# Performance work log

Hardware: AMD Instinct MI355X
Metric: run time of the kernel (lower is better)

The kernel has to match this reference:

```python
import jax, jax.numpy as jnp
import numpy as np

B, N, D, F, L, R = 16, 1024, 256, 128, 2, 2


def setup_inputs() -> dict:
    key = jax.random.key(0)
    ks = jax.random.split(key, 12)
    s = 0.05
    return {
        "node_embed": jax.random.normal(ks[0], (B, N, D), jnp.float32),
        "input_x": jax.random.normal(ks[1], (B, F), jnp.float32),
        "adj": jax.random.randint(ks[2], (R, B, N, N), 0, 2, jnp.int32),
        "WQi_w": jax.random.normal(ks[3], (L, F, F), jnp.float32) * s,
        "WQi_b": jnp.zeros((L, F), jnp.float32),
        "WQ_w": jax.random.normal(ks[4], (L, D + F, D), jnp.float32) * s,
        "WQ_b": jnp.zeros((L, D), jnp.float32),
        "WK_w": jax.random.normal(ks[5], (L, R, D + F, D), jnp.float32) * s,
        "WK_b": jnp.zeros((L, R, D), jnp.float32),
        "WV_w": jax.random.normal(ks[6], (L, R, D + F, D), jnp.float32) * s,
        "WV_b": jnp.zeros((L, R, D), jnp.float32),
        "WF_w": jax.random.normal(ks[7], (L, R * D, D), jnp.float32) * s,
        "WF_b": jnp.zeros((L, D), jnp.float32),
        "ln_g": jnp.ones((L, D), jnp.float32),
        "ln_b": jnp.zeros((L, D), jnp.float32),
    }


def _layer_norm(x, g, b, eps=1e-5):
    mu = jnp.mean(x, axis=-1, keepdims=True)
    var = jnp.var(x, axis=-1, keepdims=True)
    return (x - mu) * jax.lax.rsqrt(var + eps) * g + b


def reference(node_embed, input_x, adj, WQi_w, WQi_b, WQ_w, WQ_b,
              WK_w, WK_b, WV_w, WV_b, WF_w, WF_b, ln_g, ln_b):
    scale = 1.0 / (D ** 0.5)
    h = node_embed
    for l in range(L):
        # input feature projection, broadcast over nodes
        x1 = input_x @ WQi_w[l] + WQi_b[l]              # (B, F)
        x1 = jnp.broadcast_to(x1[:, None, :], (h.shape[0], h.shape[1], F))
        qc = jnp.concatenate([h, x1], axis=-1)          # (B, N, D+F)
        q = qc @ WQ_w[l] + WQ_b[l]                      # (B, N, D)
        outs = []
        for r in range(R):
            k = qc @ WK_w[l, r] + WK_b[l, r]            # (B, N, D)
            v = qc @ WV_w[l, r] + WV_b[l, r]            # (B, N, D)
            scores = jnp.einsum('bnd,bmd->bnm', q, k) * scale
            scores = jnp.where(adj[r] == 0, -1e9, scores)
            alpha = jax.nn.softmax(scores, axis=-1)
            outs.append(jnp.einsum('bnm,bmd->bnd', alpha, v))
        h_concat = jnp.concatenate(outs, axis=-1)       # (B, N, R*D)
        h_fused = jax.nn.relu(h_concat @ WF_w[l] + WF_b[l])
        h = _layer_norm(h + h_fused, ln_g[l], ln_b[l])
    return h
```

## Files before the change

kernel.cpp:

```cpp
#include <hip/hip_runtime.h>
#include <hip/hip_bf16.h>

#define BB 16
#define NN 1024
#define DD 256
#define FF_ 128
#define LL 2
#define RR 2
#define DF 384
#define MM (BB*NN)
#define NPROJ 1280
#define PK 768

typedef __attribute__((ext_vector_type(8))) short s16x8;
typedef __attribute__((ext_vector_type(4))) float f32x4;
typedef __attribute__((ext_vector_type(4))) unsigned short us16x4;

__device__ __forceinline__ unsigned short f2bf(float f){
  unsigned u = __builtin_bit_cast(unsigned, f);
  u += 0x7fff + ((u >> 16) & 1);
  return (unsigned short)(u >> 16);
}

__device__ __forceinline__ void gload16(const void* g, void* l){
  __builtin_amdgcn_global_load_lds(
      (const __attribute__((address_space(1))) unsigned int*)g,
      (__attribute__((address_space(3))) unsigned int*)l, 16, 0, 0);
}

#define MFMA16(a,b,c) __builtin_amdgcn_mfma_f32_16x16x32_bf16((a),(b),(c),0,0,0)

__global__ __launch_bounds__(256) void pack_adj(const int* __restrict__ adj,
                                                unsigned long long* __restrict__ bits){
  int w = threadIdx.x >> 6, lane = threadIdx.x & 63;
  size_t row = (size_t)blockIdx.x * 4 + w;
  const int* a = adj + row * NN;
  unsigned long long* brow = bits + row * 16;
  #pragma unroll
  for (int j = 0; j < 16; ++j){
    unsigned long long m = __ballot(a[j*64 + lane] != 0);
    if (lane == 0) brow[j] = m;
  }
}

#define PREP_WT   3840
#define PREP_WTF  1024
#define PREP_BALL 10
#define PREP_X1   16
#define PREP_H    2048
#define PREP_TOT  (PREP_WT+PREP_WTF+PREP_BALL+PREP_X1+PREP_H)

__global__ __launch_bounds__(256) void prep(
    const float* __restrict__ node, const float* __restrict__ inx,
    const float* __restrict__ WQi_w, const float* __restrict__ WQi_b,
    const float* __restrict__ WQ_w, const float* __restrict__ WK_w,
    const float* __restrict__ WV_w, const float* __restrict__ WQ_b,
    const float* __restrict__ WK_b, const float* __restrict__ WV_b,
    const float* __restrict__ WF_w,
    unsigned short* __restrict__ wtall, unsigned short* __restrict__ wtf,
    float* __restrict__ ball, unsigned short* __restrict__ x1bf,
    unsigned short* __restrict__ hbf){
  int bid = blockIdx.x, t = threadIdx.x;
  if (bid < PREP_WT){
    int o = bid*256 + t;
    int l = o / (NPROJ*DF); int oo = o - l*(NPROJ*DF);
    int n = oo / DF, k = oo - n*DF;
    const float* WQ = WQ_w + (size_t)l*DF*256;
    const float* WK = WK_w + (size_t)l*RR*DF*256;
    const float* WV = WV_w + (size_t)l*RR*DF*256;
    float v;
    if (n < 256)      v = WQ[(size_t)k*256 + n];
    else if (n < 768) v = WK[(size_t)((n-256)>>8)*(DF*256) + (size_t)k*256 + ((n-256)&255)];
    else              v = WV[(size_t)((n-768)>>8)*(DF*256) + (size_t)k*256 + ((n-768)&255)];
    wtall[o] = f2bf(v);
  } else if (bid < PREP_WT + PREP_WTF){
    int o = (bid - PREP_WT)*256 + t;
    int l = o >> 17; int oo = o & 131071;
    int n = oo >> 9, k = oo & 511;
    wtf[o] = f2bf(WF_w[(size_t)l*512*256 + (size_t)k*256 + n]);
  } else if (bid < PREP_WT + PREP_WTF + PREP_BALL){
    int o = (bid - PREP_WT - PREP_WTF)*256 + t;
    if (o < 2*NPROJ){
      int l = o / NPROJ, n = o - l*NPROJ;
      float v = (n < 256) ? WQ_b[l*256 + n]
              : (n < 768) ? WK_b[(size_t)l*512 + (n-256)]
                          : WV_b[(size_t)l*512 + (n-768)];
      ball[o] = v;
    }
  } else if (bid < PREP_WT + PREP_WTF + PREP_BALL + PREP_X1){
    int o = (bid - PREP_WT - PREP_WTF - PREP_BALL)*256 + t;
    int l = o >> 11, bj = o & 2047;
    int b = bj >> 7, j = bj & 127;
    const float* w = WQi_w + (size_t)l*FF_*FF_;
    float s = WQi_b[l*FF_ + j];
    for (int i = 0; i < FF_; ++i) s += inx[b*FF_ + i] * w[i*FF_ + j];
    x1bf[o] = f2bf(s);
  } else {
    int o = (bid - (PREP_TOT - PREP_H))*256 + t;
    const float4* src = (const float4*)node + (size_t)o*2;
    float4 a = src[0], c = src[1];
    uint4 pk;
    pk.x = (unsigned)f2bf(a.x) | ((unsigned)f2bf(a.y) << 16);
    pk.y = (unsigned)f2bf(a.z) | ((unsigned)f2bf(a.w) << 16);
    pk.z = (unsigned)f2bf(c.x) | ((unsigned)f2bf(c.y) << 16);
    pk.w = (unsigned)f2bf(c.z) | ((unsigned)f2bf(c.w) << 16);
    *(uint4*)(hbf + (size_t)o*8) = pk;
  }
}

__global__ __launch_bounds__(256) void gemm_big(const unsigned short* __restrict__ hbf,
    const unsigned short* __restrict__ x1l, const unsigned short* __restrict__ Wt,
    const float* __restrict__ bias, unsigned short* __restrict__ POUT,
    unsigned short* __restrict__ vtall){
  __shared__ unsigned short As[2][128*32];
  __shared__ unsigned short Bs[2][128*32];
  int t = threadIdx.x, lane = t & 63, w = t >> 6;
  int wr = w >> 1, wc = w & 1, l15 = lane & 15, lhi = lane >> 4;
  int bm = blockIdx.x, bn = blockIdx.y, bb = bm >> 3;
  f32x4 acc[4][4];
  #pragma unroll
  for (int m = 0; m < 4; ++m)
    #pragma unroll
    for (int n = 0; n < 4; ++n) acc[m][n] = (f32x4){0.f,0.f,0.f,0.f};

  auto STAGE = [&](int bi, int kk){
    #pragma unroll
    for (int i = 0; i < 2; ++i){
      int base = w*2048 + i*1024;
      int off = base + lane*16;
      int row = off >> 6, cb = off & 63;
      const char* asrc = (kk < 8)
        ? (const char*)hbf + ((size_t)(bm*128 + row)*256 + kk*32)*2 + cb
        : (const char*)x1l + ((size_t)bb*128 + (kk-8)*32)*2 + cb;
      gload16(asrc, (char*)As[bi] + base);
      gload16((const char*)Wt + ((size_t)(bn*128 + row)*DF + kk*32)*2 + cb,
              (char*)Bs[bi] + base);
    }
  };

  STAGE(0, 0);
  __syncthreads();
  for (int kk = 0; kk < 12; ++kk){
    int cur = kk & 1;
    if (kk + 1 < 12) STAGE(cur ^ 1, kk + 1);
    s16x8 af[4], bfr[4];
    #pragma unroll
    for (int m = 0; m < 4; ++m) af[m]  = *(const s16x8*)&As[cur][(wr*64 + m*16 + l15)*32 + lhi*8];
    #pragma unroll
    for (int n = 0; n < 4; ++n) bfr[n] = *(const s16x8*)&Bs[cur][(wc*64 + n*16 + l15)*32 + lhi*8];
    __builtin_amdgcn_s_setprio(1);
    #pragma unroll
    for (int m = 0; m < 4; ++m)
      #pragma unroll
      for (int n = 0; n < 4; ++n)
        acc[m][n] = MFMA16(af[m], bfr[n], acc[m][n]);
    __builtin_amdgcn_s_setprio(0);
    __syncthreads();
  }

  if (bn < 6){
    #pragma unroll
    for (int n = 0; n < 4; ++n){
      int gn = bn*128 + wc*64 + n*16 + l15;
      float bv = bias[gn];
      #pragma unroll
      for (int m = 0; m < 4; ++m){
        int gm = bm*128 + wr*64 + m*16 + lhi*4;
        #pragma unroll
        for (int i = 0; i < 4; ++i)
          POUT[(size_t)(gm + i)*PK + gn] = f2bf(acc[m][n][i] + bv);
      }
    }
  } else {
    #pragma unroll
    for (int n = 0; n < 4; ++n){
      int gn = bn*128 + wc*64 + n*16 + l15;
      float bv = bias[gn];
      int rv = gn - 768;
      int r = rv >> 8, d = rv & 255;
      #pragma unroll
      for (int m = 0; m < 4; ++m){
        int mb = (bm & 7)*128 + wr*64 + m*16 + lhi*4;
        us16x4 pk;
        #pragma unroll
        for (int i = 0; i < 4; ++i) pk[i] = f2bf(acc[m][n][i] + bv);
        *(us16x4*)(vtall + ((size_t)((r*16 + bb)*256 + d))*NN + mb) = pk;
      }
    }
  }
}

__global__ __launch_bounds__(512, 2) void attn2(const unsigned short* __restrict__ P,
    const unsigned short* __restrict__ VT, const unsigned long long* __restrict__ bits,
    unsigned short* __restrict__ hc){
  __shared__ unsigned short Kt[2][64*256];
  __shared__ unsigned short Vt[2][256*64];
  __shared__ unsigned short Pl[8][16*68];
  int t = threadIdx.x, lane = t & 63, w = t >> 6, l15 = lane & 15, lhi = lane >> 4;
  int F = blockIdx.x;
  int xcd = F & 7, j = F >> 3;
  int qt = j & 7;
  int gidx = xcd*4 + (j >> 3);
  int b = gidx & 15, r = gidx >> 4;
  const float C = 0.09016844f;

  size_t kcol = 256 + (size_t)r*256;
  const unsigned short* Vb = VT + ((size_t)(r*16 + b))*256*NN;

  s16x8 qf[8];
  {
    int qrow = qt*128 + w*16 + l15;
    const unsigned short* qp = P + ((size_t)(b*NN + qrow))*PK + lhi*8;
    #pragma unroll
    for (int dc = 0; dc < 8; ++dc) qf[dc] = *(const s16x8*)(qp + dc*32);
  }

  f32x4 acc[16];
  #pragma unroll
  for (int i = 0; i < 16; ++i) acc[i] = (f32x4){0.f,0.f,0.f,0.f};
  float mrow[4] = {-3e38f,-3e38f,-3e38f,-3e38f};
  float lrow[4] = {0.f,0.f,0.f,0.f};
  size_t bitrow = ((size_t)(r*BB + b))*NN + qt*128 + w*16 + lhi*4;

  auto STAGE = [&](int bi, int kt){
    #pragma unroll
    for (int i = 0; i < 4; ++i){
      int base = w*4096 + i*1024;
      int off = base + lane*16;
      int row = off >> 9, cb = off & 511;
      int scb = cb ^ ((row & 7) << 4);
      gload16((const char*)P + ((size_t)(b*NN + kt*64 + row)*PK + kcol)*2 + scb,
              (char*)Kt[bi] + base);
    }
    #pragma unroll
    for (int i = 0; i < 4; ++i){
      int base = w*4096 + i*1024;
      int off = base + lane*16;
      int row = off >> 7, cb = off & 127;
      int scb = cb ^ ((row & 7) << 4);
      gload16((const char*)Vb + ((size_t)row*NN + kt*64)*2 + scb,
              (char*)Vt[bi] + base);
    }
  };

  STAGE(0, 0);
  __syncthreads();

  for (int kt = 0; kt < 16; ++kt){
    int cur = kt & 1;
    if (kt + 1 < 16) STAGE(cur ^ 1, kt + 1);

    f32x4 sf[4];
    #pragma unroll
    for (int ks = 0; ks < 4; ++ks){
      sf[ks] = (f32x4){0.f,0.f,0.f,0.f};
      int krow = ks*16 + l15;
      __builtin_amdgcn_s_setprio(1);
      #pragma unroll
      for (int dc = 0; dc < 8; ++dc){
        int bo = krow*512 + (((dc*32 + lhi*8)*2) ^ ((krow & 7) << 4));
        s16x8 kf = *(const s16x8*)((const char*)Kt[cur] + bo);
        sf[ks] = MFMA16(qf[dc], kf, sf[ks]);
      }
      __builtin_amdgcn_s_setprio(0);
    }

    unsigned short* pw = &Pl[w][0];
    #pragma unroll
    for (int i = 0; i < 4; ++i){
      unsigned long long mwv = bits[(bitrow + i)*16 + kt];
      float sv[4]; float tm = -3e38f;
      #pragma unroll
      for (int ks = 0; ks < 4; ++ks){
        float s = sf[ks][i] * C;
        bool on = (mwv >> (ks*16 + l15)) & 1ULL;
        s = on ? s : -1.443e9f;
        sv[ks] = s;
        tm = fmaxf(tm, s);
      }
      #pragma unroll
      for (int xm = 1; xm < 16; xm <<= 1) tm = fmaxf(tm, __shfl_xor(tm, xm));
      float mn = mrow[i];
      if (tm > mn + 11.6f){
        float f = exp2f(mn - tm);
        mrow[i] = tm; mn = tm;
        lrow[i] *= f;
        #pragma unroll
        for (int dt = 0; dt < 16; ++dt) acc[dt][i] *= f;
      }
      float rs = 0.f;
      #pragma unroll
      for (int ks = 0; ks < 4; ++ks){
        float e = exp2f(sv[ks] - mn);
        pw[(lhi*4 + i)*68 + ks*16 + l15] = f2bf(e);
        rs += e;
      }
      #pragma unroll
      for (int xm = 1; xm < 16; xm <<= 1) rs += __shfl_xor(rs, xm);
      lrow[i] += rs;
    }

    s16x8 pa[2];
    #pragma unroll
    for (int kc = 0; kc < 2; ++kc)
      pa[kc] = *(const s16x8*)&pw[l15*68 + kc*32 + lhi*8];

    __builtin_amdgcn_s_setprio(1);
    #pragma unroll
    for (int dt = 0; dt < 16; ++dt){
      int vrow = dt*16 + l15;
      #pragma unroll
      for (int kc = 0; kc < 2; ++kc){
        int bo = vrow*128 + (((kc*32 + lhi*8)*2) ^ ((vrow & 7) << 4));
        s16x8 vf = *(const s16x8*)((const char*)Vt[cur] + bo);
        acc[dt] = MFMA16(pa[kc], vf, acc[dt]);
      }
    }
    __builtin_amdgcn_s_setprio(0);

    __syncthreads();
  }

  #pragma unroll
  for (int i = 0; i < 4; ++i){
    float inv = 1.f / lrow[i];
    int q = qt*128 + w*16 + lhi*4 + i;
    unsigned short* hrow = hc + ((size_t)(b*NN + q))*(RR*DD) + r*DD;
    #pragma unroll
    for (int dt = 0; dt < 16; ++dt)
      hrow[dt*16 + l15] = f2bf(acc[dt][i] * inv);
  }
}

__global__ __launch_bounds__(256) void gemm_ff(const unsigned short* __restrict__ A,
    const unsigned short* __restrict__ Wt, const float* __restrict__ bias,
    float* __restrict__ out){
  __shared__ unsigned short As[2][128*32];
  __shared__ unsigned short Bs[2][128*32];
  int t = threadIdx.x, lane = t & 63, w = t >> 6;
  int wr = w >> 1, wc = w & 1, l15 = lane & 15, lhi = lane >> 4;
  int bm = blockIdx.x, bn = blockIdx.y;
  f32x4 acc[4][4];
  #pragma unroll
  for (int m = 0; m < 4; ++m)
    #pragma unroll
    for (int n = 0; n < 4; ++n) acc[m][n] = (f32x4){0.f,0.f,0.f,0.f};

  auto STAGE = [&](int bi, int kk){
    #pragma unroll
    for (int i = 0; i < 2; ++i){
      int base = w*2048 + i*1024;
      int off = base + lane*16;
      int row = off >> 6, cb = off & 63;
      gload16((const char*)A  + ((size_t)(bm*128 + row)*512 + kk*32)*2 + cb,
              (char*)As[bi] + base);
      gload16((const char*)Wt + ((size_t)(bn*128 + row)*512 + kk*32)*2 + cb,
              (char*)Bs[bi] + base);
    }
  };

  STAGE(0, 0);
  __syncthreads();
  for (int kk = 0; kk < 16; ++kk){
    int cur = kk & 1;
    if (kk + 1 < 16) STAGE(cur ^ 1, kk + 1);
    s16x8 af[4], bfr[4];
    #pragma unroll
    for (int m = 0; m < 4; ++m) af[m]  = *(const s16x8*)&As[cur][(wr*64 + m*16 + l15)*32 + lhi*8];
    #pragma unroll
    for (int n = 0; n < 4; ++n) bfr[n] = *(const s16x8*)&Bs[cur][(wc*64 + n*16 + l15)*32 + lhi*8];
    __builtin_amdgcn_s_setprio(1);
    #pragma unroll
    for (int m = 0; m < 4; ++m)
      #pragma unroll
      for (int n = 0; n < 4; ++n)
        acc[m][n] = MFMA16(af[m], bfr[n], acc[m][n]);
    __builtin_amdgcn_s_setprio(0);
    __syncthreads();
  }

  #pragma unroll
  for (int n = 0; n < 4; ++n){
    int gn = bn*128 + wc*64 + n*16 + l15;
    float bv = bias[gn];
    #pragma unroll
    for (int m = 0; m < 4; ++m){
      int gm = bm*128 + wr*64 + m*16 + lhi*4;
      #pragma unroll
      for (int i = 0; i < 4; ++i)
        out[(size_t)(gm + i)*DD + gn] = acc[m][n][i] + bv;
    }
  }
}

template<int WRITEH>
__global__ __launch_bounds__(256) void ln_res2(const float* __restrict__ ff,
    const float* __restrict__ hin, const float* __restrict__ g,
    const float* __restrict__ bv, float* __restrict__ hout,
    unsigned short* __restrict__ hbf){
  int w = threadIdx.x >> 6, lane = threadIdx.x & 63;
  size_t row = (size_t)blockIdx.x * 4 + w;
  f32x4 fv = *(const f32x4*)(ff  + row*DD + lane*4);
  f32x4 hv = *(const f32x4*)(hin + row*DD + lane*4);
  float x[4], s = 0.f, ss = 0.f;
  #pragma unroll
  for (int j = 0; j < 4; ++j){ x[j] = fmaxf(fv[j], 0.f) + hv[j]; s += x[j]; ss += x[j]*x[j]; }
  #pragma unroll
  for (int xm = 1; xm < 64; xm <<= 1){ s += __shfl_xor(s, xm); ss += __shfl_xor(ss, xm); }
  float mu = s * (1.f/256.f);
  float var = ss * (1.f/256.f) - mu*mu;
  float rstd = rsqrtf(var + 1e-5f);
  f32x4 o;
  #pragma unroll
  for (int j = 0; j < 4; ++j){ int c = lane*4 + j; o[j] = (x[j]-mu)*rstd*g[c] + bv[c]; }
  *(f32x4*)(hout + row*DD + lane*4) = o;
  if (WRITEH){
    uint2 pv;
    pv.x = (unsigned)f2bf(o[0]) | ((unsigned)f2bf(o[1]) << 16);
    pv.y = (unsigned)f2bf(o[2]) | ((unsigned)f2bf(o[3]) << 16);
    *(uint2*)(hbf + row*DD + lane*4) = pv;
  }
}

extern "C" void kernel_launch(void* const* d_in, const int* in_sizes, int n_in,
                              void* d_out, int out_size, void* d_ws, size_t ws_size,
                              hipStream_t stream){
  (void)in_sizes; (void)n_in; (void)out_size; (void)ws_size;
  const float* node  = (const float*)d_in[0];
  const float* inx   = (const float*)d_in[1];
  const int*   adj   = (const int*)d_in[2];
  const float* WQi_w = (const float*)d_in[3];
  const float* WQi_b = (const float*)d_in[4];
  const float* WQ_w  = (const float*)d_in[5];
  const float* WQ_b  = (const float*)d_in[6];
  const float* WK_w  = (const float*)d_in[7];
  const float* WK_b  = (const float*)d_in[8];
  const float* WV_w  = (const float*)d_in[9];
  const float* WV_b  = (const float*)d_in[10];
  const float* WF_w  = (const float*)d_in[11];
  const float* WF_b  = (const float*)d_in[12];
  const float* ln_g  = (const float*)d_in[13];
  const float* ln_b  = (const float*)d_in[14];
  float* hout = (float*)d_out;

  char* wsp = (char*)d_ws;
  auto alloc = [&](size_t n){ char* p = wsp; wsp += (n + 255) & ~(size_t)255; return p; };
  unsigned long long* bits = (unsigned long long*)alloc((size_t)RR*BB*NN*16*8);
  unsigned short* wtall = (unsigned short*)alloc((size_t)2*NPROJ*DF*2);
  unsigned short* wtf   = (unsigned short*)alloc((size_t)2*DD*512*2);
  float*          ball  = (float*)alloc((size_t)2*NPROJ*4);
  unsigned short* x1bf  = (unsigned short*)alloc((size_t)2*BB*FF_*2);
  unsigned short* hbf   = (unsigned short*)alloc((size_t)MM*DD*2);
  unsigned short* POUT  = (unsigned short*)alloc((size_t)MM*PK*2);
  unsigned short* vtall = (unsigned short*)alloc((size_t)RR*BB*DD*NN*2);
  unsigned short* hc    = (unsigned short*)alloc((size_t)MM*512*2);
  float*          ffo   = (float*)alloc((size_t)MM*DD*4);

  pack_adj<<<RR*BB*NN/4, 256, 0, stream>>>(adj, bits);
  prep<<<PREP_TOT, 256, 0, stream>>>(node, inx, WQi_w, WQi_b, WQ_w, WK_w, WV_w,
                                     WQ_b, WK_b, WV_b, WF_w,
                                     wtall, wtf, ball, x1bf, hbf);

  for (int l = 0; l < LL; ++l){
    gemm_big<<<dim3(128,10), 256, 0, stream>>>(hbf, x1bf + (size_t)l*BB*FF_,
        wtall + (size_t)l*NPROJ*DF, ball + (size_t)l*NPROJ, POUT, vtall);

    attn2<<<256, 512, 0, stream>>>(POUT, vtall, bits, hc);

    gemm_ff<<<dim3(128,2), 256, 0, stream>>>(hc, wtf + (size_t)l*DD*512, WF_b + l*DD, ffo);

    if (l == 0) ln_res2<1><<<MM/4, 256, 0, stream>>>(ffo, node, ln_g, ln_b, hout, hbf);
    else        ln_res2<0><<<MM/4, 256, 0, stream>>>(ffo, (const float*)hout,
                                                     ln_g + DD, ln_b + DD, hout, nullptr);
  }
}
```

Baseline: 315.9 us.

## Restructure attention kernel into 2-wave blocks with 32 query rows per wave

Replaces the 8-wave, 128-query attention block with a 2-wave block that handles 64 queries, each wave processing two 16-row query slabs. Every K and V fragment read from LDS now feeds two MFMAs, which halves LDS read traffic per flop. It also drops K/V double buffering (single buffer with two barriers per tile), removes the s_setprio hints, and adds an XOR swizzle to the P staging buffer. Doubling the accumulator registers and serialising loads with compute may reduce occupancy and latency hiding, and the grid doubles to 512 blocks.

New measurement: 443.3 us. +40.3%, slower.

```diff
diff --git a/kernel.cpp b/kernel.cpp
--- a/kernel.cpp
+++ b/kernel.cpp
@@ -190,146 +190,149 @@
   }
 }
 
-__global__ __launch_bounds__(512, 2) void attn2(const unsigned short* __restrict__ P,
+__global__ __launch_bounds__(128, 1) void attn3(const unsigned short* __restrict__ P,
     const unsigned short* __restrict__ VT, const unsigned long long* __restrict__ bits,
     unsigned short* __restrict__ hc){
-  __shared__ unsigned short Kt[2][64*256];
-  __shared__ unsigned short Vt[2][256*64];
-  __shared__ unsigned short Pl[8][16*68];
+  __shared__ unsigned short Kt[64*256];
+  __shared__ unsigned short Vt[256*64];
+  __shared__ unsigned short Pl[2][32*64];
   int t = threadIdx.x, lane = t & 63, w = t >> 6, l15 = lane & 15, lhi = lane >> 4;
   int F = blockIdx.x;
   int xcd = F & 7, j = F >> 3;
-  int qt = j & 7;
-  int gidx = xcd*4 + (j >> 3);
+  int qt = j & 15;
+  int gidx = xcd*4 + (j >> 4);
   int b = gidx & 15, r = gidx >> 4;
   const float C = 0.09016844f;
 
   size_t kcol = 256 + (size_t)r*256;
   const unsigned short* Vb = VT + ((size_t)(r*16 + b))*256*NN;
 
-  s16x8 qf[8];
-  {
-    int qrow = qt*128 + w*16 + l15;
+  s16x8 qf[2][8];
+  #pragma unroll
+  for (int qs = 0; qs < 2; ++qs){
+    int qrow = qt*64 + w*32 + qs*16 + l15;
     const unsigned short* qp = P + ((size_t)(b*NN + qrow))*PK + lhi*8;
     #pragma unroll
-    for (int dc = 0; dc < 8; ++dc) qf[dc] = *(const s16x8*)(qp + dc*32);
-  }
-
-  f32x4 acc[16];
-  #pragma unroll
-  for (int i = 0; i < 16; ++i) acc[i] = (f32x4){0.f,0.f,0.f,0.f};
-  float mrow[4] = {-3e38f,-3e38f,-3e38f,-3e38f};
-  float lrow[4] = {0.f,0.f,0.f,0.f};
-  size_t bitrow = ((size_t)(r*BB + b))*NN + qt*128 + w*16 + lhi*4;
-
-  auto STAGE = [&](int bi, int kt){
-    #pragma unroll
-    for (int i = 0; i < 4; ++i){
-      int base = w*4096 + i*1024;
+    for (int dc = 0; dc < 8; ++dc) qf[qs][dc] = *(const s16x8*)(qp + dc*32);
+  }
+
+  f32x4 acc[2][16];
+  #pragma unroll
+  for (int qs = 0; qs < 2; ++qs)
+    #pragma unroll
+    for (int i = 0; i < 16; ++i) acc[qs][i] = (f32x4){0.f,0.f,0.f,0.f};
+  float mrow[2][4] = {{-3e38f,-3e38f,-3e38f,-3e38f},{-3e38f,-3e38f,-3e38f,-3e38f}};
+  float lrow[2][4] = {{0.f,0.f,0.f,0.f},{0.f,0.f,0.f,0.f}};
+  size_t bitbase = ((size_t)(r*BB + b))*NN + qt*64 + w*32;
+
+  for (int kt = 0; kt < 16; ++kt){
+    __syncthreads();
+    #pragma unroll
+    for (int i = 0; i < 16; ++i){
+      int base = w*16384 + i*1024;
       int off = base + lane*16;
       int row = off >> 9, cb = off & 511;
       int scb = cb ^ ((row & 7) << 4);
       gload16((const char*)P + ((size_t)(b*NN + kt*64 + row)*PK + kcol)*2 + scb,
-              (char*)Kt[bi] + base);
-    }
-    #pragma unroll
-    for (int i = 0; i < 4; ++i){
-      int base = w*4096 + i*1024;
+              (char*)Kt + base);
+    }
+    #pragma unroll
+    for (int i = 0; i < 16; ++i){
+      int base = w*16384 + i*1024;
       int off = base + lane*16;
       int row = off >> 7, cb = off & 127;
       int scb = cb ^ ((row & 7) << 4);
       gload16((const char*)Vb + ((size_t)row*NN + kt*64)*2 + scb,
-              (char*)Vt[bi] + base);
-    }
-  };
-
-  STAGE(0, 0);
-  __syncthreads();
-
-  for (int kt = 0; kt < 16; ++kt){
-    int cur = kt & 1;
-    if (kt + 1 < 16) STAGE(cur ^ 1, kt + 1);
-
-    f32x4 sf[4];
+              (char*)Vt + base);
+    }
+    __syncthreads();
+
+    f32x4 sf[2][4];
     #pragma unroll
     for (int ks = 0; ks < 4; ++ks){
-      sf[ks] = (f32x4){0.f,0.f,0.f,0.f};
+      sf[0][ks] = (f32x4){0.f,0.f,0.f,0.f};
+      sf[1][ks] = (f32x4){0.f,0.f,0.f,0.f};
       int krow = ks*16 + l15;
-      __builtin_amdgcn_s_setprio(1);
       #pragma unroll
       for (int dc = 0; dc < 8; ++dc){
         int bo = krow*512 + (((dc*32 + lhi*8)*2) ^ ((krow & 7) << 4));
-        s16x8 kf = *(const s16x8*)((const char*)Kt[cur] + bo);
-        sf[ks] = MFMA16(qf[dc], kf, sf[ks]);
-      }
-      __builtin_amdgcn_s_setprio(0);
-    }
-
-    unsigned short* pw = &Pl[w][0];
-    #pragma unroll
-    for (int i = 0; i < 4; ++i){
-      unsigned long long mwv = bits[(bitrow + i)*16 + kt];
-      float sv[4]; float tm = -3e38f;
-      #pragma unroll
-      for (int ks = 0; ks < 4; ++ks){
-        float s = sf[ks][i] * C;
-        bool on = (mwv >> (ks*16 + l15)) & 1ULL;
-        s = on ? s : -1.443e9f;
-        sv[ks] = s;
-        tm = fmaxf(tm, s);
-      }
-      #pragma unroll
-      for (int xm = 1; xm < 16; xm <<= 1) tm = fmaxf(tm, __shfl_xor(tm, xm));
-      float mn = mrow[i];
-      if (tm > mn + 11.6f){
-        float f = exp2f(mn - tm);
-        mrow[i] = tm; mn = tm;
-        lrow[i] *= f;
-        #pragma unroll
-        for (int dt = 0; dt < 16; ++dt) acc[dt][i] *= f;
-      }
-      float rs = 0.f;
-      #pragma unroll
-      for (int ks = 0; ks < 4; ++ks){
-        float e = exp2f(sv[ks] - mn);
-        pw[(lhi*4 + i)*68 + ks*16 + l15] = f2bf(e);
-        rs += e;
-      }
-      #pragma unroll
-      for (int xm = 1; xm < 16; xm <<= 1) rs += __shfl_xor(rs, xm);
-      lrow[i] += rs;
-    }
-
-    s16x8 pa[2];
-    #pragma unroll
-    for (int kc = 0; kc < 2; ++kc)
-      pa[kc] = *(const s16x8*)&pw[l15*68 + kc*32 + lhi*8];
-
-    __builtin_amdgcn_s_setprio(1);
+        s16x8 kf = *(const s16x8*)((const char*)Kt + bo);
+        sf[0][ks] = MFMA16(qf[0][dc], kf, sf[0][ks]);
+        sf[1][ks] = MFMA16(qf[1][dc], kf, sf[1][ks]);
+      }
+    }
+
+    #pragma unroll
+    for (int qs = 0; qs < 2; ++qs){
+      #pragma unroll
+      for (int i = 0; i < 4; ++i){
+        unsigned long long mwv = bits[(bitbase + qs*16 + lhi*4 + i)*16 + kt];
+        float sv[4]; float tm = -3e38f;
+        #pragma unroll
+        for (int ks = 0; ks < 4; ++ks){
+          float s = sf[qs][ks][i] * C;
+          bool on = (mwv >> (ks*16 + l15)) & 1ULL;
+          s = on ? s : -1.443e9f;
+          sv[ks] = s;
+          tm = fmaxf(tm, s);
+        }
+        #pragma unroll
+        for (int xm = 1; xm < 16; xm <<= 1) tm = fmaxf(tm, __shfl_xor(tm, xm));
+        float mn = mrow[qs][i];
+        if (tm > mn + 11.6f){
+          float f = exp2f(mn - tm);
+          mrow[qs][i] = tm; mn = tm;
+          lrow[qs][i] *= f;
+          #pragma unroll
+          for (int dt = 0; dt < 16; ++dt) acc[qs][dt][i] *= f;
+        }
+        int prow = qs*16 + lhi*4 + i;
+        float rs = 0.f;
+        #pragma unroll
+        for (int ks = 0; ks < 4; ++ks){
+          float e = exp2f(sv[ks] - mn);
+          Pl[w][prow*64 + ((ks*16 + l15) ^ ((prow & 7) << 3))] = f2bf(e);
+          rs += e;
+        }
+        #pragma unroll
+        for (int xm = 1; xm < 16; xm <<= 1) rs += __shfl_xor(rs, xm);
+        lrow[qs][i] += rs;
+      }
+    }
+
+    s16x8 pa[2][2];
+    #pragma unroll
+    for (int qs = 0; qs < 2; ++qs)
+      #pragma unroll
+      for (int kc = 0; kc < 2; ++kc){
+        int prow = qs*16 + l15;
+        pa[qs][kc] = *(const s16x8*)&Pl[w][prow*64 + ((kc*32 + lhi*8) ^ ((prow & 7) << 3))];
+      }
+
     #pragma unroll
     for (int dt = 0; dt < 16; ++dt){
       int vrow = dt*16 + l15;
       #pragma unroll
       for (int kc = 0; kc < 2; ++kc){
         int bo = vrow*128 + (((kc*32 + lhi*8)*2) ^ ((vrow & 7) << 4));
-        s16x8 vf = *(const s16x8*)((const char*)Vt[cur] + bo);
-        acc[dt] = MFMA16(pa[kc], vf, acc[dt]);
-      }
-    }
-    __builtin_amdgcn_s_setprio(0);
-
-    __syncthreads();
-  }
-
-  #pragma unroll
-  for (int i = 0; i < 4; ++i){
-    float inv = 1.f / lrow[i];
-    int q = qt*128 + w*16 + lhi*4 + i;
-    unsigned short* hrow = hc + ((size_t)(b*NN + q))*(RR*DD) + r*DD;
-    #pragma unroll
-    for (int dt = 0; dt < 16; ++dt)
-      hrow[dt*16 + l15] = f2bf(acc[dt][i] * inv);
-  }
+        s16x8 vf = *(const s16x8*)((const char*)Vt + bo);
+        acc[0][dt] = MFMA16(pa[0][kc], vf, acc[0][dt]);
+        acc[1][dt] = MFMA16(pa[1][kc], vf, acc[1][dt]);
+      }
+    }
+  }
+
+  #pragma unroll
+  for (int qs = 0; qs < 2; ++qs)
+    #pragma unroll
+    for (int i = 0; i < 4; ++i){
+      float inv = 1.f / lrow[qs][i];
+      int q = qt*64 + w*32 + qs*16 + lhi*4 + i;
+      unsigned short* hrow = hc + ((size_t)(b*NN + q))*(RR*DD) + r*DD;
+      #pragma unroll
+      for (int dt = 0; dt < 16; ++dt)
+        hrow[dt*16 + l15] = f2bf(acc[qs][dt][i] * inv);
+    }
 }
 
 __global__ __launch_bounds__(256) void gemm_ff(const unsigned short* __restrict__ A,
@@ -465,7 +468,7 @@
     gemm_big<<<dim3(128,10), 256, 0, stream>>>(hbf, x1bf + (size_t)l*BB*FF_,
         wtall + (size_t)l*NPROJ*DF, ball + (size_t)l*NPROJ, POUT, vtall);
 
-    attn2<<<256, 512, 0, stream>>>(POUT, vtall, bits, hc);
+    attn3<<<512, 128, 0, stream>>>(POUT, vtall, bits, hc);
 
     gemm_ff<<<dim3(128,2), 256, 0, stream>>>(hc, wtf + (size_t)l*DD*512, WF_b + l*DD, ffo);
 
```
